# Kernel optimization log

Measured on AMD Instinct MI355X. Metric: run time of the kernel, lower is better.

Reference implementation:

```python
import jax, jax.numpy as jnp
import numpy as np

BIG_NUMBER = 1e7   # repo constant used to mask padded adjacency slots
MAX_ITERS = 32     # params['flow_iters']


def _build_graph(B, N, D, valid_deg, seed=0):
    """Random d-regular-ish graph: each valid slot d holds a permutation of nodes,
    so every node has exactly `valid_deg` in-edges. in_indices[b,v,d] = (b,u,s)
    such that adj[b,u,s] == v. Padded slots (d >= valid_deg) hold the sentinel N
    and their in_indices point to a padded (near-zero-weight) flow entry."""
    rng = np.random.default_rng(seed)
    adj = np.full((B, N, D), N, dtype=np.int32)
    in_idx = np.zeros((B, N, D, 3), dtype=np.int32)
    in_idx[..., 0] = np.arange(B, dtype=np.int32)[:, None, None]
    in_idx[..., 2] = valid_deg  # padded slots -> flow[b, 0, valid_deg] (weight ~ 0)
    for b in range(B):
        for d in range(valid_deg):
            perm = rng.permutation(N).astype(np.int32)
            adj[b, :, d] = perm                      # edge u -> perm[u] via slot d
            inv = np.argsort(perm).astype(np.int32)  # inv[v] = u with perm[u] == v
            in_idx[b, :, d, 1] = inv
            in_idx[b, :, d, 2] = d
    return jnp.asarray(adj), jnp.asarray(in_idx)


def setup_inputs():
    B, N, D, VALID = 4, 100000, 16, 12
    key = jax.random.key(0)
    k1, k2 = jax.random.split(key)
    adj_lst, in_indices = _build_graph(B, N, D, VALID)
    return {
        "flow_proportions": jax.random.normal(k1, (B, N, D), dtype=jnp.float32),
        "demands": jax.random.normal(k2, (B, N, 1), dtype=jnp.float32),
        "adj_lst": adj_lst,
        "in_indices": in_indices,
        "num_nodes": N,
    }


def reference(flow_proportions, demands, adj_lst, in_indices, num_nodes):
    # --- masked softmax over neighbor slots (padded slots get -BIG_NUMBER) ---
    mask = (adj_lst == num_nodes).astype(flow_proportions.dtype)   # [B,N,D]
    masked = flow_proportions - BIG_NUMBER * mask
    weights = jax.nn.softmax(masked, axis=-1)                      # normalized_weights

    # --- mcf_solver: iterate flow <- weights * relu(inflow - demand) ---
    bidx = in_indices[..., 0]   # [B,N,D] batch index
    src = in_indices[..., 1]    # [B,N,D] source node of d-th in-edge
    slot = in_indices[..., 2]   # [B,N,D] slot of this node in source's adj list

    def step(flow, _):
        # gather incoming edge flows, sum -> inflow per node [B,N,1]
        inflow = flow[bidx, src, slot].sum(axis=-1, keepdims=True)
        new_flow = weights * jax.nn.relu(inflow - demands)
        return new_flow, None

    flow, _ = jax.lax.scan(step, jnp.zeros_like(weights), None, length=MAX_ITERS)
    # flow_cost (loss) = sum over nodes/slots of cost_fn(flow) = flow**2 here:
    # flow_cost = jnp.sum(flow * flow, axis=(1, 2))
    return flow
```

## Files before the change

kernel.cpp:

```cpp
#include <hip/hip_runtime.h>

#define DEG 16
#define E12 12
#define MAX_ITERS 32
#define BLK 1024
#define LDSF 25600
#define JMAX 96

__device__ __forceinline__ float ld_sc0(const float* p) {
    return __hip_atomic_load((float*)p, __ATOMIC_RELAXED, __HIP_MEMORY_SCOPE_AGENT);
}
__device__ __forceinline__ void st_sc0(float* p, float v) {
    __hip_atomic_store(p, v, __ATOMIC_RELAXED, __HIP_MEMORY_SCOPE_AGENT);
}
__device__ __forceinline__ unsigned ld_u32_sc0(const unsigned* p) {
    return __hip_atomic_load((unsigned*)p, __ATOMIC_RELAXED, __HIP_MEMORY_SCOPE_AGENT);
}
__device__ __forceinline__ void st_u32_sc0(unsigned* p, unsigned v) {
    __hip_atomic_store(p, v, __ATOMIC_RELAXED, __HIP_MEMORY_SCOPE_AGENT);
}

__device__ __forceinline__ int get_xcd() {
    unsigned x;
    asm volatile("s_getreg_b32 %0, hwreg(HW_REG_XCC_ID)" : "=s"(x));
    return (int)(x & 7u);
}

__device__ __forceinline__ void grid_barrier(unsigned* cnt, unsigned* gen,
                                             unsigned target, unsigned nblocks) {
    __syncthreads();
    if (threadIdx.x == 0) {
        __threadfence();
        unsigned arrived = __hip_atomic_fetch_add(cnt, 1u, __ATOMIC_ACQ_REL,
                                                  __HIP_MEMORY_SCOPE_AGENT);
        if (arrived == nblocks - 1u) {
            __hip_atomic_store(cnt, 0u, __ATOMIC_RELAXED, __HIP_MEMORY_SCOPE_AGENT);
            __hip_atomic_fetch_add(gen, 1u, __ATOMIC_RELEASE, __HIP_MEMORY_SCOPE_AGENT);
        } else {
            while (__hip_atomic_load(gen, __ATOMIC_RELAXED,
                                     __HIP_MEMORY_SCOPE_AGENT) < target)
                __builtin_amdgcn_s_sleep(2);
        }
        __threadfence();
    }
    __syncthreads();
}

__device__ __forceinline__ void xcd_barrier(unsigned* cnt, unsigned* gen,
                                            unsigned target, unsigned nblocks) {
    __syncthreads();
    if (threadIdx.x == 0) {
        unsigned arrived = __hip_atomic_fetch_add(cnt, 1u, __ATOMIC_RELEASE,
                                                  __HIP_MEMORY_SCOPE_WORKGROUP);
        if (arrived == nblocks - 1u) {
            __hip_atomic_store(cnt, 0u, __ATOMIC_RELAXED,
                               __HIP_MEMORY_SCOPE_WORKGROUP);
            __hip_atomic_fetch_add(gen, 1u, __ATOMIC_RELEASE,
                                   __HIP_MEMORY_SCOPE_WORKGROUP);
        } else {
            while (ld_u32_sc0(gen) < target)
                __builtin_amdgcn_s_sleep(2);
        }
    }
    __syncthreads();
}

__device__ __forceinline__ void softmax_row(const float* __restrict__ fp,
                                            const int* __restrict__ adj,
                                            float* __restrict__ wout,
                                            size_t base, int N) {
    const float4* f4 = (const float4*)(fp + base);
    const int4*   a4 = (const int4*)(adj + base);
    float v[DEG];
#pragma unroll
    for (int k = 0; k < DEG / 4; ++k) {
        float4 f = f4[k];
        int4   a = a4[k];
        v[4*k+0] = (a.x == N) ? f.x - 1e7f : f.x;
        v[4*k+1] = (a.y == N) ? f.y - 1e7f : f.y;
        v[4*k+2] = (a.z == N) ? f.z - 1e7f : f.z;
        v[4*k+3] = (a.w == N) ? f.w - 1e7f : f.w;
    }
    float m = v[0];
#pragma unroll
    for (int j = 1; j < DEG; ++j) m = fmaxf(m, v[j]);
    float s = 0.f;
#pragma unroll
    for (int j = 0; j < DEG; ++j) { v[j] = __expf(v[j] - m); s += v[j]; }
    float inv = 1.f / s;
    float4* w4 = (float4*)(wout + base);
#pragma unroll
    for (int k = 0; k < DEG / 4; ++k) {
        float4 o;
        o.x = v[4*k+0] * inv;
        o.y = v[4*k+1] * inv;
        o.z = v[4*k+2] * inv;
        o.w = v[4*k+3] * inv;
        w4[k] = o;
    }
}

__device__ __forceinline__ float node_acc12(const int* __restrict__ es,
                                            const float* __restrict__ ew,
                                            const float* __restrict__ Rc) {
    const int4*   s4 = (const int4*)es;
    const float4* w4 = (const float4*)ew;
    int4 a = s4[0], b = s4[1], c = s4[2];
    float4 x = w4[0], y = w4[1], z = w4[2];
    float acc;
    acc  = x.x * Rc[a.x];  acc += x.y * Rc[a.y];
    acc += x.z * Rc[a.z];  acc += x.w * Rc[a.w];
    acc += y.x * Rc[b.x];  acc += y.y * Rc[b.y];
    acc += y.z * Rc[b.z];  acc += y.w * Rc[b.w];
    acc += z.x * Rc[c.x];  acc += z.y * Rc[c.y];
    acc += z.z * Rc[c.z];  acc += z.w * Rc[c.w];
    return acc;
}

__device__ __forceinline__ void scale_row(float* __restrict__ wout, int g, float r) {
    float4* w4 = (float4*)(wout + (size_t)g * DEG);
#pragma unroll
    for (int k = 0; k < DEG / 4; ++k) {
        float4 v = w4[k];
        v.x *= r; v.y *= r; v.z *= r; v.w *= r;
        w4[k] = v;
    }
}

__global__ __launch_bounds__(BLK, 4)
void fused7_k(const float* __restrict__ fp, const int* __restrict__ adj,
              const int* __restrict__ in_idx, const float* __restrict__ dem,
              const int* __restrict__ nn, float* __restrict__ wout,
              char* __restrict__ wsb, int nodes) {
    __shared__ float lds[LDSF];
    __shared__ int s_xcd, s_rank, s_mode, s_part, s_jbad;
    __shared__ int s_cm[4];
    __shared__ int s_off[5];

    unsigned* g_cnt  = (unsigned*)(wsb);
    unsigned* g_gen  = (unsigned*)(wsb + 128);
    unsigned* blkcnt = (unsigned*)(wsb + 2304);
    unsigned* ovf    = (unsigned*)(wsb + 2432);
    unsigned* jovf   = (unsigned*)(wsb + 2436);
    int*   e_src   = (int*)(wsb + 4096);
    float* e_w     = (float*)(wsb + 4096 + (size_t)nodes * E12 * 4);
    float* Rf0     = (float*)((char*)e_w + (size_t)nodes * E12 * 4);
    float* Rf1     = Rf0 + nodes;
    float* slices  = Rf1 + nodes;
    uint2* regions = (uint2*)((char*)(slices) + (size_t)nodes * 16);

    const int N   = *nn;
    const int tid = (int)threadIdx.x;
    const int T   = (int)gridDim.x * BLK;
    const unsigned nblocks = gridDim.x;
    unsigned gb = 0;

    if (tid == 0) {
        int x = get_xcd();
        s_xcd  = x;
        s_rank = (int)__hip_atomic_fetch_add(&blkcnt[x], 1u, __ATOMIC_RELAXED,
                                             __HIP_MEMORY_SCOPE_AGENT);
    }
    __syncthreads();
    const int my_xcd  = s_xcd;
    const int my_rank = s_rank;

#pragma unroll
    for (int rep = 0; rep < 2; ++rep) {
        int g = (int)blockIdx.x * BLK + tid + rep * T;
        if (g < nodes) softmax_row(fp, adj, wout, (size_t)g * DEG, N);
    }
    grid_barrier(g_cnt, g_gen, ++gb, nblocks);

#pragma unroll
    for (int rep = 0; rep < 2; ++rep) {
        int g = (int)blockIdx.x * BLK + tid + rep * T;
        if (g >= nodes) continue;
        const int gbat = g / N;
        const int4* t4 = (const int4*)(in_idx + (size_t)g * 48);
        int cb[16], cs[16], cl[16];
#pragma unroll
        for (int q = 0; q < 4; ++q) {
            int4 qa = t4[3*q + 0];
            int4 qb = t4[3*q + 1];
            int4 qc = t4[3*q + 2];
            cb[4*q+0] = qa.x; cs[4*q+0] = qa.y; cl[4*q+0] = qa.z;
            cb[4*q+1] = qa.w; cs[4*q+1] = qb.x; cl[4*q+1] = qb.y;
            cb[4*q+2] = qb.z; cs[4*q+2] = qb.w; cl[4*q+2] = qc.x;
            cb[4*q+3] = qc.y; cs[4*q+3] = qc.z; cl[4*q+3] = qc.w;
        }
        float cw[16];
#pragma unroll
        for (int k = 0; k < 16; ++k)
            cw[k] = wout[((size_t)cb[k] * N + cs[k]) * DEG + cl[k]];
        bool bad = (cw[12] != 0.f) || (cw[13] != 0.f) ||
                   (cw[14] != 0.f) || (cw[15] != 0.f);
#pragma unroll
        for (int k = 0; k < E12; ++k)
            bad = bad || (cb[k] != gbat) || ((unsigned)cs[k] >= (unsigned)N);
        if (bad) st_u32_sc0(ovf, 1u);
        int4*   es4 = (int4*)(e_src + (size_t)g * E12);
        float4* ew4 = (float4*)(e_w + (size_t)g * E12);
        es4[0] = make_int4(cs[0], cs[1], cs[2], cs[3]);
        es4[1] = make_int4(cs[4], cs[5], cs[6], cs[7]);
        es4[2] = make_int4(cs[8], cs[9], cs[10], cs[11]);
        ew4[0] = make_float4(cw[0], cw[1], cw[2], cw[3]);
        ew4[1] = make_float4(cw[4], cw[5], cw[6], cw[7]);
        ew4[2] = make_float4(cw[8], cw[9], cw[10], cw[11]);
    }
    grid_barrier(g_cnt, g_gen, ++gb, nblocks);

    const int npb   = (N + 31) >> 5;
    const int nch   = (N + LDSF - 1) / LDSF;
    const int chunk = (N + nch - 1) / nch;
    if (tid == 0) {
        unsigned cc[8];
#pragma unroll
        for (int x = 0; x < 8; ++x) cc[x] = ld_u32_sc0(&blkcnt[x]);
        bool ok = (4 * N == nodes) && (N > 0) && (npb <= 4 * BLK) &&
                  (nch >= 1) && (nch <= 4) && (chunk <= LDSF) &&
                  (ld_u32_sc0(ovf) == 0u);
#pragma unroll
        for (int p = 0; p < 4; ++p)
            ok = ok && (cc[2*p] >= 32u || cc[2*p+1] >= 32u);
        s_mode = ok ? 1 : 0;
        s_part = (ok && cc[my_xcd] >= 32u && my_rank < 32) ? 1 : 0;
    }
    __syncthreads();
    const bool fast = (s_mode == 1);
    const bool part = (s_part == 1);

    if (fast) {
        const int batch = my_xcd >> 1;
        const int lbase = my_rank * npb;
        const int lim   = min(lbase + npb, N);
        float d[4];
        int   lno[4];
        bool  act[4];
        float r[4];
        uint2* reg = regions + (size_t)(my_xcd * 32 + my_rank) * (JMAX * BLK);

        if (part) {
            if (tid < 4) s_cm[tid] = 0;
            __syncthreads();
            const int b1 = chunk, b2 = 2 * chunk, b3 = 3 * chunk;
            int c0 = 0, c1 = 0, c2 = 0, c3 = 0;
#pragma unroll
            for (int s = 0; s < 4; ++s) {
                int l = lbase + s * BLK + tid;
                lno[s] = l;
                act[s] = (l < lim);
                d[s] = 0.f;
                if (act[s]) {
                    int g = batch * N + l;
                    d[s] = dem[g];
                    const int* es = e_src + (size_t)g * E12;
#pragma unroll
                    for (int k = 0; k < E12; ++k) {
                        int src = es[k];
                        int c = (src >= b1) + (src >= b2) + (src >= b3);
                        c0 += (c == 0); c1 += (c == 1);
                        c2 += (c == 2); c3 += (c == 3);
                    }
                }
            }
            atomicMax(&s_cm[0], c0); atomicMax(&s_cm[1], c1);
            atomicMax(&s_cm[2], c2); atomicMax(&s_cm[3], c3);
            __syncthreads();
            if (tid == 0) {
                s_off[0] = 0;
                s_off[1] = s_cm[0];
                s_off[2] = s_cm[0] + s_cm[1];
                s_off[3] = s_cm[0] + s_cm[1] + s_cm[2];
                s_off[4] = s_cm[0] + s_cm[1] + s_cm[2] + s_cm[3];
                if (s_off[4] > JMAX) st_u32_sc0(jovf, 1u);
            }
            __syncthreads();
            if (s_off[4] <= JMAX) {
                int cur0 = s_off[0], cur1 = s_off[1],
                    cur2 = s_off[2], cur3 = s_off[3];
#pragma unroll
                for (int s = 0; s < 4; ++s) {
                    if (!act[s]) continue;
                    int g = batch * N + lno[s];
                    const int*   es = e_src + (size_t)g * E12;
                    const float* ew = e_w + (size_t)g * E12;
#pragma unroll
                    for (int k = 0; k < E12; ++k) {
                        int src = es[k];
                        float w = ew[k];
                        int c = (src >= b1) + (src >= b2) + (src >= b3);
                        int j = (c == 0) ? cur0 : (c == 1) ? cur1
                               : (c == 2) ? cur2 : cur3;
                        reg[(size_t)j * BLK + tid] =
                            make_uint2((unsigned)src | ((unsigned)s << 20),
                                       __float_as_uint(w));
                        cur0 += (c == 0); cur1 += (c == 1);
                        cur2 += (c == 2); cur3 += (c == 3);
                    }
                }
                int curs[1];
                (void)curs;
                {
                    int cc_[4] = {cur0, cur1, cur2, cur3};
#pragma unroll
                    for (int c = 0; c < 4; ++c) {
                        unsigned ps = (unsigned)(c * chunk);
                        for (int j = cc_[c]; j < s_off[c + 1]; ++j)
                            reg[(size_t)j * BLK + tid] = make_uint2(ps, 0u);
                    }
                }
            }
        }
        grid_barrier(g_cnt, g_gen, ++gb, nblocks);
        if (tid == 0) s_jbad = (int)ld_u32_sc0(jovf);
        __syncthreads();

        if (s_jbad == 0) {
            if (!part) return;
            unsigned* xc = (unsigned*)(wsb + 256 + my_xcd * 256);
            unsigned* xg = (unsigned*)(wsb + 256 + my_xcd * 256 + 128);
            unsigned xb = 0;
            float* bufA = slices + (size_t)(2 * my_xcd + 0) * N;
            float* bufB = slices + (size_t)(2 * my_xcd + 1) * N;

#pragma unroll
            for (int s = 0; s < 4; ++s) {
                r[s] = fmaxf(-d[s], 0.f);
                if (act[s]) st_sc0(bufA + lno[s], r[s]);
            }
            xcd_barrier(xc, xg, ++xb, 32u);

            float* Rin  = bufA;
            float* Rout = bufB;
            for (int t = 1; t < MAX_ITERS; ++t) {
                float a0 = 0.f, a1 = 0.f, a2 = 0.f, a3 = 0.f;
                for (int c = 0; c < nch; ++c) {
                    const int cbase = c * chunk;
                    const int ce = min(chunk, N - cbase);
                    for (int i = tid; i < ce; i += BLK)
                        lds[i] = ld_sc0(Rin + cbase + i);
                    __syncthreads();
                    const int jb = s_off[c], je = s_off[c + 1];
                    for (int j = jb; j < je; ++j) {
                        uint2 pr = reg[(size_t)j * BLK + tid];
                        float w = __uint_as_float(pr.y);
                        int idx = (int)(pr.x & 0xFFFFFu) - cbase;
                        int tg  = (int)(pr.x >> 20);
                        float wv = w * lds[idx];
                        a0 += (tg == 0) ? wv : 0.f;
                        a1 += (tg == 1) ? wv : 0.f;
                        a2 += (tg == 2) ? wv : 0.f;
                        a3 += (tg == 3) ? wv : 0.f;
                    }
                    __syncthreads();
                }
                r[0] = fmaxf(a0 - d[0], 0.f);
                r[1] = fmaxf(a1 - d[1], 0.f);
                r[2] = fmaxf(a2 - d[2], 0.f);
                r[3] = fmaxf(a3 - d[3], 0.f);
                if (t < MAX_ITERS - 1) {
#pragma unroll
                    for (int s = 0; s < 4; ++s)
                        if (act[s]) st_sc0(Rout + lno[s], r[s]);
                    xcd_barrier(xc, xg, ++xb, 32u);
                    float* tmp = Rin; Rin = Rout; Rout = tmp;
                }
            }
#pragma unroll
            for (int s = 0; s < 4; ++s)
                if (act[s]) scale_row(wout, batch * N + lno[s], r[s]);
            return;
        }
    }

    {
        int g0 = (int)blockIdx.x * BLK + tid;
        int g1 = g0 + T;
        bool a0 = (g0 < nodes), a1 = (g1 < nodes);
        float d0 = a0 ? dem[g0] : 0.f;
        float d1 = a1 ? dem[g1] : 0.f;
        int base0 = a0 ? (g0 / N) * N : 0;
        int base1 = a1 ? (g1 / N) * N : 0;
        float r0 = fmaxf(-d0, 0.f), r1 = fmaxf(-d1, 0.f);
        if (a0) Rf0[g0] = r0;
        if (a1) Rf0[g1] = r1;
        grid_barrier(g_cnt, g_gen, ++gb, nblocks);
        const float* Rc = Rf0;
        float*       Rn = Rf1;
        for (int t = 1; t < MAX_ITERS; ++t) {
            if (a0) r0 = fmaxf(node_acc12(e_src + (size_t)g0 * E12,
                                          e_w + (size_t)g0 * E12,
                                          Rc + base0) - d0, 0.f);
            if (a1) r1 = fmaxf(node_acc12(e_src + (size_t)g1 * E12,
                                          e_w + (size_t)g1 * E12,
                                          Rc + base1) - d1, 0.f);
            if (t < MAX_ITERS - 1) {
                if (a0) Rn[g0] = r0;
                if (a1) Rn[g1] = r1;
                grid_barrier(g_cnt, g_gen, ++gb, nblocks);
                float* tmp = (float*)Rc; Rc = Rn; Rn = tmp;
            }
        }
        if (a0) scale_row(wout, g0, r0);
        if (a1) scale_row(wout, g1, r1);
    }
}

__global__ void softmax_k(const float* __restrict__ fp, const int* __restrict__ adj,
                          const int* __restrict__ nn, float* __restrict__ wout,
                          int nodes) {
    int i = blockIdx.x * blockDim.x + threadIdx.x;
    if (i >= nodes) return;
    softmax_row(fp, adj, wout, (size_t)i * DEG, *nn);
}

__global__ void gather_k(const int* __restrict__ in_idx, const float* __restrict__ w,
                         const int* __restrict__ nn, int* __restrict__ e_srcO,
                         float* __restrict__ e_wO, int edges) {
    int e = blockIdx.x * blockDim.x + threadIdx.x;
    if (e >= edges) return;
    const int N = *nn;
    size_t e3 = 3 * (size_t)e;
    int fi = in_idx[e3] * N + in_idx[e3 + 1];
    e_srcO[e] = fi;
    e_wO[e]   = w[(size_t)fi * DEG + in_idx[e3 + 2]];
}

__global__ void iter_k(const int* __restrict__ e_srcO, const float* __restrict__ e_wO,
                       const float* __restrict__ dem, const float* __restrict__ Rin,
                       float* __restrict__ Rout, int nodes) {
    int i = blockIdx.x * blockDim.x + threadIdx.x;
    if (i >= nodes) return;
    const size_t base = (size_t)i * DEG;
    const int4*   s4 = (const int4*)(e_srcO + base);
    const float4* w4 = (const float4*)(e_wO + base);
    float acc = 0.f;
#pragma unroll
    for (int k = 0; k < DEG / 4; ++k) {
        int4   s = s4[k];
        float4 w = w4[k];
        acc += w.x * Rin[s.x];
        acc += w.y * Rin[s.y];
        acc += w.z * Rin[s.z];
        acc += w.w * Rin[s.w];
    }
    float r = acc - dem[i];
    Rout[i] = r > 0.f ? r : 0.f;
}

__global__ void final_k(const float* __restrict__ w, const float* __restrict__ R,
                        float* __restrict__ out, int nodes) {
    int i = blockIdx.x * blockDim.x + threadIdx.x;
    if (i >= nodes) return;
    scale_row((float*)w, i, R[i]);
    (void)out;
}

extern "C" void kernel_launch(void* const* d_in, const int* in_sizes, int n_in,
                              void* d_out, int out_size, void* d_ws, size_t ws_size,
                              hipStream_t stream) {
    const float* fp  = (const float*)d_in[0];
    const float* dem = (const float*)d_in[1];
    const int*   adj = (const int*)d_in[2];
    const int*   idx = (const int*)d_in[3];
    const int*   nn  = (const int*)d_in[4];

    const int edges = in_sizes[0];
    const int nodes = in_sizes[1];

    float* weights = (float*)d_out;
    char*  ws      = (char*)d_ws;

    int dev = 0, cus = 0, maxBlk = 0;
    hipGetDevice(&dev);
    hipDeviceGetAttribute(&cus, hipDeviceAttributeMultiprocessorCount, dev);
    hipOccupancyMaxActiveBlocksPerMultiprocessor(&maxBlk, (const void*)fused7_k,
                                                 BLK, 0);

    const size_t need = 4096 + (size_t)nodes * (E12 * 8 + 8 + 16)
                      + (size_t)256 * JMAX * BLK * 8;
    const int grid = cus;

    const bool fused_ok = (maxBlk >= 1) && (cus >= 16) &&
                          ((long long)grid * BLK * 2 >= nodes) &&
                          (ws_size >= need) && (nodes % 4 == 0);

    if (fused_ok) {
        hipMemsetAsync(ws, 0, 4096, stream);
        void* args[] = { (void*)&fp, (void*)&adj, (void*)&idx, (void*)&dem,
                         (void*)&nn, (void*)&weights, (void*)&ws, (void*)&nodes };
        hipLaunchCooperativeKernel((const void*)fused7_k, dim3(grid), dim3(BLK),
                                   args, 0, stream);
    } else {
        int*   e_srcO = (int*)ws;
        float* e_wO   = (float*)(ws + (size_t)edges * sizeof(int));
        float* R0     = (float*)(ws + (size_t)edges * 8);
        float* R1     = R0 + nodes;
        const int blk = 256;
        const int gn = (nodes + blk - 1) / blk;
        const int ge = (edges + blk - 1) / blk;
        hipMemsetAsync(R0, 0, (size_t)nodes * sizeof(float), stream);
        softmax_k<<<gn, blk, 0, stream>>>(fp, adj, nn, weights, nodes);
        gather_k<<<ge, blk, 0, stream>>>(idx, weights, nn, e_srcO, e_wO, edges);
        float* a = R0;
        float* b = R1;
        for (int t = 0; t < MAX_ITERS; ++t) {
            iter_k<<<gn, blk, 0, stream>>>(e_srcO, e_wO, dem, a, b, nodes);
            float* tmp = a; a = b; b = tmp;
        }
        final_k<<<gn, blk, 0, stream>>>(weights, a, (float*)d_out, nodes);
    }
}
```

Baseline: 1.024 ms.

## Replace per-thread padded edge regions with chunk-sorted edge stream and LDS accumulation

The per-thread padded edge lists (JMAX slots per thread, where every thread walks the maximum count for each chunk) are replaced by a compact per-block edge stream sorted by source chunk. Edges are processed cooperatively by all threads, and each product is accumulated into per-destination LDS slots with shared-memory atomicAdd. This removes the padding and warp divergence of the old layout and also drops the extra grid barrier and the JMAX overflow fallback. In exchange it adds LDS atomic contention, and float atomics make the summation order nondeterministic.

```diff
diff --git a/kernel.cpp b/kernel.cpp
--- a/kernel.cpp
+++ b/kernel.cpp
@@ -4,8 +4,8 @@
 #define E12 12
 #define MAX_ITERS 32
 #define BLK 1024
-#define LDSF 25600
-#define JMAX 96
+#define CHF 25000
+#define NPBMAX 4096
 
 __device__ __forceinline__ float ld_sc0(const float* p) {
     return __hip_atomic_load((float*)p, __ATOMIC_RELAXED, __HIP_MEMORY_SCOPE_AGENT);
@@ -128,26 +128,25 @@
 }
 
 __global__ __launch_bounds__(BLK, 4)
-void fused7_k(const float* __restrict__ fp, const int* __restrict__ adj,
+void fused8_k(const float* __restrict__ fp, const int* __restrict__ adj,
               const int* __restrict__ in_idx, const float* __restrict__ dem,
               const int* __restrict__ nn, float* __restrict__ wout,
               char* __restrict__ wsb, int nodes) {
-    __shared__ float lds[LDSF];
-    __shared__ int s_xcd, s_rank, s_mode, s_part, s_jbad;
-    __shared__ int s_cm[4];
-    __shared__ int s_off[5];
+    __shared__ float ldsChunk[CHF];
+    __shared__ float accL[NPBMAX];
+    __shared__ int s_xcd, s_rank, s_mode, s_part;
+    __shared__ int s_cnt[4], s_cur[4], s_offE[5];
 
     unsigned* g_cnt  = (unsigned*)(wsb);
     unsigned* g_gen  = (unsigned*)(wsb + 128);
     unsigned* blkcnt = (unsigned*)(wsb + 2304);
     unsigned* ovf    = (unsigned*)(wsb + 2432);
-    unsigned* jovf   = (unsigned*)(wsb + 2436);
-    int*   e_src   = (int*)(wsb + 4096);
-    float* e_w     = (float*)(wsb + 4096 + (size_t)nodes * E12 * 4);
-    float* Rf0     = (float*)((char*)e_w + (size_t)nodes * E12 * 4);
-    float* Rf1     = Rf0 + nodes;
-    float* slices  = Rf1 + nodes;
-    uint2* regions = (uint2*)((char*)(slices) + (size_t)nodes * 16);
+    int*   e_src  = (int*)(wsb + 4096);
+    float* e_w    = (float*)(wsb + 4096 + (size_t)nodes * E12 * 4);
+    float* Rf0    = (float*)((char*)e_w + (size_t)nodes * E12 * 4);
+    float* Rf1    = Rf0 + nodes;
+    float* slices = Rf1 + nodes;
+    uint2* streams = (uint2*)((char*)slices + (size_t)nodes * 16);
 
     const int N   = *nn;
     const int tid = (int)threadIdx.x;
@@ -211,15 +210,15 @@
     grid_barrier(g_cnt, g_gen, ++gb, nblocks);
 
     const int npb   = (N + 31) >> 5;
-    const int nch   = (N + LDSF - 1) / LDSF;
-    const int chunk = (N + nch - 1) / nch;
+    const int nch   = (N + CHF - 1) / CHF;
+    const int chunk = (nch > 0) ? (N + nch - 1) / nch : 1;
     if (tid == 0) {
         unsigned cc[8];
 #pragma unroll
         for (int x = 0; x < 8; ++x) cc[x] = ld_u32_sc0(&blkcnt[x]);
-        bool ok = (4 * N == nodes) && (N > 0) && (npb <= 4 * BLK) &&
-                  (nch >= 1) && (nch <= 4) && (chunk <= LDSF) &&
-                  (ld_u32_sc0(ovf) == 0u);
+        bool ok = (4 * N == nodes) && (N > 0) && (npb <= NPBMAX) &&
+                  (nch >= 1) && (nch <= 4) && (chunk <= CHF) &&
+                  (chunk < 32768) && (ld_u32_sc0(ovf) == 0u);
 #pragma unroll
         for (int p = 0; p < 4; ++p)
             ok = ok && (cc[2*p] >= 32u || cc[2*p+1] >= 32u);
@@ -227,151 +226,105 @@
         s_part = (ok && cc[my_xcd] >= 32u && my_rank < 32) ? 1 : 0;
     }
     __syncthreads();
-    const bool fast = (s_mode == 1);
-    const bool part = (s_part == 1);
-
-    if (fast) {
+
+    if (s_mode == 1) {
+        if (s_part != 1) return;
         const int batch = my_xcd >> 1;
-        const int lbase = my_rank * npb;
-        const int lim   = min(lbase + npb, N);
-        float d[4];
-        int   lno[4];
-        bool  act[4];
-        float r[4];
-        uint2* reg = regions + (size_t)(my_xcd * 32 + my_rank) * (JMAX * BLK);
-
-        if (part) {
-            if (tid < 4) s_cm[tid] = 0;
-            __syncthreads();
-            const int b1 = chunk, b2 = 2 * chunk, b3 = 3 * chunk;
-            int c0 = 0, c1 = 0, c2 = 0, c3 = 0;
-#pragma unroll
-            for (int s = 0; s < 4; ++s) {
-                int l = lbase + s * BLK + tid;
-                lno[s] = l;
-                act[s] = (l < lim);
-                d[s] = 0.f;
-                if (act[s]) {
-                    int g = batch * N + l;
-                    d[s] = dem[g];
-                    const int* es = e_src + (size_t)g * E12;
-#pragma unroll
-                    for (int k = 0; k < E12; ++k) {
-                        int src = es[k];
-                        int c = (src >= b1) + (src >= b2) + (src >= b3);
-                        c0 += (c == 0); c1 += (c == 1);
-                        c2 += (c == 2); c3 += (c == 3);
-                    }
+        const int lb = my_rank * npb;
+        const int le = min(lb + npb, N);
+        uint2* stream = streams + (size_t)(my_xcd * 32 + my_rank) * (NPBMAX * E12);
+
+        if (tid < 4) { s_cnt[tid] = 0; }
+        __syncthreads();
+        int   myl[4];  bool mya[4];  float d[4];
+#pragma unroll
+        for (int s = 0; s < 4; ++s) {
+            int l = lb + s * BLK + tid;
+            myl[s] = l; mya[s] = (l < le); d[s] = 0.f;
+            if (mya[s]) {
+                d[s] = dem[batch * N + l];
+                const int* es = e_src + (size_t)(batch * N + l) * E12;
+#pragma unroll
+                for (int k = 0; k < E12; ++k)
+                    atomicAdd(&s_cnt[es[k] / chunk], 1);
+            }
+        }
+        __syncthreads();
+        if (tid == 0) {
+            s_offE[0] = 0;
+#pragma unroll
+            for (int c = 0; c < 4; ++c) s_offE[c + 1] = s_offE[c] + s_cnt[c];
+#pragma unroll
+            for (int c = 0; c < 4; ++c) s_cur[c] = s_offE[c];
+        }
+        __syncthreads();
+#pragma unroll
+        for (int s = 0; s < 4; ++s) {
+            if (!mya[s]) continue;
+            int g = batch * N + myl[s];
+            const int*   es = e_src + (size_t)g * E12;
+            const float* ew = e_w + (size_t)g * E12;
+            int dst = myl[s] - lb;
+#pragma unroll
+            for (int k = 0; k < E12; ++k) {
+                int src = es[k];
+                int c = src / chunk;
+                int pos = atomicAdd(&s_cur[c], 1);
+                stream[pos] = make_uint2(((unsigned)dst << 15) |
+                                         (unsigned)(src - c * chunk),
+                                         __float_as_uint(ew[k]));
+            }
+        }
+        __syncthreads();
+
+        unsigned* xc = (unsigned*)(wsb + 256 + my_xcd * 256);
+        unsigned* xg = (unsigned*)(wsb + 256 + my_xcd * 256 + 128);
+        unsigned xb = 0;
+        float* bufA = slices + (size_t)(2 * my_xcd + 0) * N;
+        float* bufB = slices + (size_t)(2 * my_xcd + 1) * N;
+
+        float rr[4];
+#pragma unroll
+        for (int s = 0; s < 4; ++s) {
+            rr[s] = fmaxf(-d[s], 0.f);
+            if (mya[s]) st_sc0(bufA + myl[s], rr[s]);
+        }
+        xcd_barrier(xc, xg, ++xb, 32u);
+
+        float* Rin  = bufA;
+        float* Rout = bufB;
+        for (int t = 1; t < MAX_ITERS; ++t) {
+            for (int i = tid; i < npb; i += BLK) accL[i] = 0.f;
+            for (int c = 0; c < nch; ++c) {
+                const int cbase = c * chunk;
+                const int ce = min(chunk, N - cbase);
+                for (int i = tid; i < ce; i += BLK)
+                    ldsChunk[i] = ld_sc0(Rin + cbase + i);
+                __syncthreads();
+                const int ee = s_offE[c + 1];
+                for (int e = s_offE[c] + tid; e < ee; e += BLK) {
+                    uint2 pr = stream[e];
+                    atomicAdd(&accL[pr.x >> 15],
+                              __uint_as_float(pr.y) * ldsChunk[pr.x & 0x7FFFu]);
                 }
+                __syncthreads();
             }
-            atomicMax(&s_cm[0], c0); atomicMax(&s_cm[1], c1);
-            atomicMax(&s_cm[2], c2); atomicMax(&s_cm[3], c3);
-            __syncthreads();
-            if (tid == 0) {
-                s_off[0] = 0;
-                s_off[1] = s_cm[0];
-                s_off[2] = s_cm[0] + s_cm[1];
-                s_off[3] = s_cm[0] + s_cm[1] + s_cm[2];
-                s_off[4] = s_cm[0] + s_cm[1] + s_cm[2] + s_cm[3];
-                if (s_off[4] > JMAX) st_u32_sc0(jovf, 1u);
+#pragma unroll
+            for (int s = 0; s < 4; ++s)
+                if (mya[s]) rr[s] = fmaxf(accL[myl[s] - lb] - d[s], 0.f);
+            if (t < MAX_ITERS - 1) {
+#pragma unroll
+                for (int s = 0; s < 4; ++s)
+                    if (mya[s]) st_sc0(Rout + myl[s], rr[s]);
+                xcd_barrier(xc, xg, ++xb, 32u);
+                float* tmp = Rin; Rin = Rout; Rout = tmp;
             }
-            __syncthreads();
-            if (s_off[4] <= JMAX) {
-                int cur0 = s_off[0], cur1 = s_off[1],
-                    cur2 = s_off[2], cur3 = s_off[3];
-#pragma unroll
-                for (int s = 0; s < 4; ++s) {
-                    if (!act[s]) continue;
-                    int g = batch * N + lno[s];
-                    const int*   es = e_src + (size_t)g * E12;
-                    const float* ew = e_w + (size_t)g * E12;
-#pragma unroll
-                    for (int k = 0; k < E12; ++k) {
-                        int src = es[k];
-                        float w = ew[k];
-                        int c = (src >= b1) + (src >= b2) + (src >= b3);
-                        int j = (c == 0) ? cur0 : (c == 1) ? cur1
-                               : (c == 2) ? cur2 : cur3;
-                        reg[(size_t)j * BLK + tid] =
-                            make_uint2((unsigned)src | ((unsigned)s << 20),
-                                       __float_as_uint(w));
-                        cur0 += (c == 0); cur1 += (c == 1);
-                        cur2 += (c == 2); cur3 += (c == 3);
-                    }
-                }
-                int curs[1];
-                (void)curs;
-                {
-                    int cc_[4] = {cur0, cur1, cur2, cur3};
-#pragma unroll
-                    for (int c = 0; c < 4; ++c) {
-                        unsigned ps = (unsigned)(c * chunk);
-                        for (int j = cc_[c]; j < s_off[c + 1]; ++j)
-                            reg[(size_t)j * BLK + tid] = make_uint2(ps, 0u);
-                    }
-                }
-            }
-        }
-        grid_barrier(g_cnt, g_gen, ++gb, nblocks);
-        if (tid == 0) s_jbad = (int)ld_u32_sc0(jovf);
-        __syncthreads();
-
-        if (s_jbad == 0) {
-            if (!part) return;
-            unsigned* xc = (unsigned*)(wsb + 256 + my_xcd * 256);
-            unsigned* xg = (unsigned*)(wsb + 256 + my_xcd * 256 + 128);
-            unsigned xb = 0;
-            float* bufA = slices + (size_t)(2 * my_xcd + 0) * N;
-            float* bufB = slices + (size_t)(2 * my_xcd + 1) * N;
-
-#pragma unroll
-            for (int s = 0; s < 4; ++s) {
-                r[s] = fmaxf(-d[s], 0.f);
-                if (act[s]) st_sc0(bufA + lno[s], r[s]);
-            }
-            xcd_barrier(xc, xg, ++xb, 32u);
-
-            float* Rin  = bufA;
-            float* Rout = bufB;
-            for (int t = 1; t < MAX_ITERS; ++t) {
-                float a0 = 0.f, a1 = 0.f, a2 = 0.f, a3 = 0.f;
-                for (int c = 0; c < nch; ++c) {
-                    const int cbase = c * chunk;
-                    const int ce = min(chunk, N - cbase);
-                    for (int i = tid; i < ce; i += BLK)
-                        lds[i] = ld_sc0(Rin + cbase + i);
-                    __syncthreads();
-                    const int jb = s_off[c], je = s_off[c + 1];
-                    for (int j = jb; j < je; ++j) {
-                        uint2 pr = reg[(size_t)j * BLK + tid];
-                        float w = __uint_as_float(pr.y);
-                        int idx = (int)(pr.x & 0xFFFFFu) - cbase;
-                        int tg  = (int)(pr.x >> 20);
-                        float wv = w * lds[idx];
-                        a0 += (tg == 0) ? wv : 0.f;
-                        a1 += (tg == 1) ? wv : 0.f;
-                        a2 += (tg == 2) ? wv : 0.f;
-                        a3 += (tg == 3) ? wv : 0.f;
-                    }
-                    __syncthreads();
-                }
-                r[0] = fmaxf(a0 - d[0], 0.f);
-                r[1] = fmaxf(a1 - d[1], 0.f);
-                r[2] = fmaxf(a2 - d[2], 0.f);
-                r[3] = fmaxf(a3 - d[3], 0.f);
-                if (t < MAX_ITERS - 1) {
-#pragma unroll
-                    for (int s = 0; s < 4; ++s)
-                        if (act[s]) st_sc0(Rout + lno[s], r[s]);
-                    xcd_barrier(xc, xg, ++xb, 32u);
-                    float* tmp = Rin; Rin = Rout; Rout = tmp;
-                }
-            }
-#pragma unroll
-            for (int s = 0; s < 4; ++s)
-                if (act[s]) scale_row(wout, batch * N + lno[s], r[s]);
-            return;
-        }
+        }
+
+#pragma unroll
+        for (int s = 0; s < 4; ++s)
+            if (mya[s]) scale_row(wout, batch * N + myl[s], rr[s]);
+        return;
     }
 
     {
@@ -475,11 +428,11 @@
     int dev = 0, cus = 0, maxBlk = 0;
     hipGetDevice(&dev);
     hipDeviceGetAttribute(&cus, hipDeviceAttributeMultiprocessorCount, dev);
-    hipOccupancyMaxActiveBlocksPerMultiprocessor(&maxBlk, (const void*)fused7_k,
+    hipOccupancyMaxActiveBlocksPerMultiprocessor(&maxBlk, (const void*)fused8_k,
                                                  BLK, 0);
 
     const size_t need = 4096 + (size_t)nodes * (E12 * 8 + 8 + 16)
-                      + (size_t)256 * JMAX * BLK * 8;
+                      + (size_t)256 * NPBMAX * E12 * 8;
     const int grid = cus;
 
     const bool fused_ok = (maxBlk >= 1) && (cus >= 16) &&
@@ -490,7 +443,7 @@
         hipMemsetAsync(ws, 0, 4096, stream);
         void* args[] = { (void*)&fp, (void*)&adj, (void*)&idx, (void*)&dem,
                          (void*)&nn, (void*)&weights, (void*)&ws, (void*)&nodes };
-        hipLaunchCooperativeKernel((const void*)fused7_k, dim3(grid), dim3(BLK),
+        hipLaunchCooperativeKernel((const void*)fused8_k, dim3(grid), dim3(BLK),
                                    args, 0, stream);
     } else {
         int*   e_srcO = (int*)ws;
```

After: 1.024 ms. About the same (+0.0%).
